# Optimization experiments

Hardware: AMD Instinct MI355X
Metric: run time of the kernel (lower is better)

The kernel has to match this reference:

```python
import jax, jax.numpy as jnp
import numpy as np

N_NODES = 50000
N_EDGES = 800000
IN = 128
HID = 128
OUT = 128
EDGE_F = 2
EPS = 1e-30


def _linear_params(key, fan_in, fan_out, bias=True):
    k1, k2 = jax.random.split(key)
    bound = 1.0 / np.sqrt(fan_in)
    W = jax.random.uniform(k1, (fan_in, fan_out), jnp.float32, -bound, bound)
    if bias:
        b = jax.random.uniform(k2, (fan_out,), jnp.float32, -bound, bound)
        return W, b
    return (W,)


def setup_inputs() -> dict:
    key = jax.random.key(0)
    ks = jax.random.split(key, 12)
    node_feat = jax.random.normal(ks[0], (N_NODES, IN), jnp.float32)
    coord_feat = jax.random.normal(ks[1], (N_NODES, 3), jnp.float32)
    edge_feat = jax.random.normal(ks[2], (N_EDGES, EDGE_F), jnp.float32)
    src = jax.random.randint(ks[3], (N_EDGES,), 0, N_NODES, jnp.int32)
    dst = jax.random.randint(ks[4], (N_EDGES,), 0, N_NODES, jnp.int32)
    # edge_mlp: Linear(2*IN+EDGE_F+1 -> HID), SiLU, Linear(HID -> HID), SiLU
    eW1, eb1 = _linear_params(ks[5], 2 * IN + EDGE_F + 1, HID)
    eW2, eb2 = _linear_params(ks[6], HID, HID)
    # node_mlp: Linear(IN+HID -> HID), SiLU, Linear(HID -> OUT)
    nW1, nb1 = _linear_params(ks[7], IN + HID, HID)
    nW2, nb2 = _linear_params(ks[8], HID, OUT)
    # coord_mlp: Linear(HID -> HID), SiLU, Linear(HID -> 1, bias=False)
    cW1, cb1 = _linear_params(ks[9], HID, HID)
    (cW2,) = _linear_params(ks[10], HID, 1, bias=False)
    return {
        "node_feat": node_feat, "coord_feat": coord_feat, "edge_feat": edge_feat,
        "src": src, "dst": dst,
        "eW1": eW1, "eb1": eb1, "eW2": eW2, "eb2": eb2,
        "nW1": nW1, "nb1": nb1, "nW2": nW2, "nb2": nb2,
        "cW1": cW1, "cb1": cb1, "cW2": cW2,
    }


def reference(node_feat, coord_feat, edge_feat, src, dst,
              eW1, eb1, eW2, eb2, nW1, nb1, nW2, nb2, cW1, cb1, cW2):
    silu = jax.nn.silu
    n = node_feat.shape[0]
    # per-edge gathers (src -> dst message flow, as in DGL)
    h_src = node_feat[src]                      # [E, IN]
    h_dst = node_feat[dst]                      # [E, IN]
    x_diff = coord_feat[src] - coord_feat[dst]  # [E, 3]
    radial = jnp.sum(x_diff * x_diff, axis=1, keepdims=True)  # [E, 1]
    x_diff = x_diff / (jnp.sqrt(radial) + EPS)
    # edge MLP
    f = jnp.concatenate([h_src, h_dst, radial, edge_feat], axis=-1)  # [E, 2*IN+1+EF]
    msg_h = silu(silu(f @ eW1 + eb1) @ eW2 + eb2)                    # [E, HID]
    msg_x = (silu(msg_h @ cW1 + cb1) @ cW2) * x_diff                 # [E, 3]
    # scatter to destination nodes: sum for h, mean for x
    h_neigh = jax.ops.segment_sum(msg_h, dst, num_segments=n)        # [N, HID]
    x_sum = jax.ops.segment_sum(msg_x, dst, num_segments=n)          # [N, 3]
    deg = jax.ops.segment_sum(jnp.ones((msg_x.shape[0],), msg_x.dtype), dst, num_segments=n)
    x_neigh = x_sum / jnp.maximum(deg, 1.0)[:, None]
    # node update
    h = silu(jnp.concatenate([node_feat, h_neigh], axis=-1) @ nW1 + nb1) @ nW2 + nb2
    x = coord_feat + x_neigh
    return h, x
```

## Files before the change

### kernel.cpp

```cpp
#include <hip/hip_runtime.h>
#include <hip/hip_bf16.h>

#define N_NODES 50000
#define E_TOTAL 800000
#define IN      128
#define HID     128
#define EPB     64
#define XOFF    ((size_t)N_NODES * HID)
#define FP      296
#define H1OFF   160
#define HP      136
#define CP      264

typedef __attribute__((ext_vector_type(8))) short short8v;
typedef __attribute__((ext_vector_type(4))) float f32x4;

__device__ __forceinline__ float silu_f(float x) { return x / (1.0f + __expf(-x)); }

__device__ __forceinline__ uint pkbf(float lo, float hi) {
    float2 f; f.x = lo; f.y = hi;
    __hip_bfloat162 h = __float22bfloat162_rn(f);
    union { __hip_bfloat162 h; uint u; } c; c.h = h;
    return c.u;
}

__device__ __forceinline__ ushort f2bf(float x) {
    uint u = __float_as_uint(x);
    u += 0x7fff + ((u >> 16) & 1);
    return (ushort)(u >> 16);
}

__device__ __forceinline__ float bf2f(short s) {
    return __uint_as_float(((uint)(ushort)s) << 16);
}

__global__ __launch_bounds__(256) void prep_kernel(
    const float* __restrict__ eW1, const float* __restrict__ eW2,
    const float* __restrict__ cW1, const float* __restrict__ nW1,
    const float* __restrict__ nW2, const float* __restrict__ eb1,
    const float* __restrict__ node_feat,
    ushort* __restrict__ pk1old, ushort* __restrict__ pka, ushort* __restrict__ pkb,
    ushort* __restrict__ pk2, ushort* __restrict__ pk3,
    ushort* __restrict__ pkn1, ushort* __restrict__ pkn2,
    float* __restrict__ cmb, ushort* __restrict__ nfb, int do_nfb)
{
    int id = blockIdx.x * 256 + threadIdx.x;
    if (id < 18944) {
        const float* W; ushort* dp; int K, idx;
        if (id < 4608)       { idx = id;         W = eW1;            dp = pk1old; K = 259; }
        else if (id < 6656)  { idx = id - 4608;  W = eW1;            dp = pka;    K = 128; }
        else if (id < 8704)  { idx = id - 6656;  W = eW1 + 128*128;  dp = pkb;    K = 128; }
        else if (id < 10752) { idx = id - 8704;  W = eW2;            dp = pk2;    K = 128; }
        else if (id < 12800) { idx = id - 10752; W = cW1;            dp = pk3;    K = 128; }
        else if (id < 16896) { idx = id - 12800; W = nW1;            dp = pkn1;   K = 256; }
        else                 { idx = id - 16896; W = nW2;            dp = pkn2;   K = 128; }
        int kt = idx >> 9, n = (idx >> 6) & 7, ll = idx & 63;
        int col = (n << 4) + (ll & 15);
        short8v o;
#pragma unroll
        for (int j = 0; j < 8; ++j) {
            int k = (kt << 5) + ((ll >> 4) << 3) + j;
            o[j] = (k < K) ? (short)f2bf(W[(size_t)k * 128 + col]) : (short)0;
        }
        *reinterpret_cast<short8v*>(dp + (size_t)idx * 8) = o;
    } else if (id < 19072) {
        int c = id - 18944;
        cmb[c*4+0] = eW1[256*128 + c];
        cmb[c*4+1] = eW1[257*128 + c];
        cmb[c*4+2] = eW1[258*128 + c];
        cmb[c*4+3] = eb1[c];
    } else if (do_nfb) {
        int idx = id - 19072;
        if (idx < N_NODES * 16) {
            const float4* s = reinterpret_cast<const float4*>(node_feat + (size_t)idx * 8);
            float4 a = s[0], b = s[1];
            uint4 u;
            u.x = pkbf(a.x, a.y); u.y = pkbf(a.z, a.w);
            u.z = pkbf(b.x, b.y); u.w = pkbf(b.z, b.w);
            *reinterpret_cast<uint4*>(nfb + (size_t)idx * 8) = u;
        }
    }
}

__global__ __launch_bounds__(256) void hist_kernel(
    const int* __restrict__ dst, int* __restrict__ cnt)
{
    int e = blockIdx.x * 256 + threadIdx.x;
    if (e < E_TOTAL) atomicAdd(&cnt[dst[e]], 1);
}

__global__ __launch_bounds__(1024) void scan_a(
    const int* __restrict__ cnt, int* __restrict__ part)
{
    __shared__ int ws[16];
    int t = threadIdx.x, lane = t & 63, wv = t >> 6;
    int i = blockIdx.x * 1024 + t;
    int v = (i < N_NODES) ? cnt[i] : 0;
#pragma unroll
    for (int off = 32; off >= 1; off >>= 1) v += __shfl_xor(v, off);
    if (lane == 0) ws[wv] = v;
    __syncthreads();
    if (t < 16) {
        int s = ws[t];
#pragma unroll
        for (int off = 8; off >= 1; off >>= 1) s += __shfl_xor(s, off);
        if (t == 0) part[blockIdx.x] = s;
    }
}

__global__ __launch_bounds__(64) void scan_b(int* __restrict__ part, int n)
{
    int t = threadIdx.x;
    int v = (t < n) ? part[t] : 0;
    int x = v;
#pragma unroll
    for (int off = 1; off < 64; off <<= 1) {
        int y = __shfl_up(x, off);
        if (t >= off) x += y;
    }
    if (t < n) part[t] = x - v;
}

__global__ __launch_bounds__(1024) void scan_c(
    int* __restrict__ cnt, const int* __restrict__ part, int* __restrict__ ptr2)
{
    __shared__ int ws[16];
    int t = threadIdx.x, lane = t & 63, wv = t >> 6;
    int i = blockIdx.x * 1024 + t;
    int v = (i < N_NODES) ? cnt[i] : 0;
    int x = v;
#pragma unroll
    for (int off = 1; off < 64; off <<= 1) {
        int y = __shfl_up(x, off);
        if (lane >= off) x += y;
    }
    if (lane == 63) ws[wv] = x;
    __syncthreads();
    if (t < 16) {
        int s = ws[t], xx = s;
#pragma unroll
        for (int off = 1; off < 16; off <<= 1) {
            int y = __shfl_up(xx, off);
            if (t >= off) xx += y;
        }
        ws[t] = xx - s;
    }
    __syncthreads();
    int excl = part[blockIdx.x] + ws[wv] + x - v;
    if (i < N_NODES) { cnt[i] = excl; ptr2[i] = excl; }
    if (i == N_NODES - 1) { cnt[N_NODES] = E_TOTAL; ptr2[N_NODES] = E_TOTAL; }
}

__global__ __launch_bounds__(256) void scatter_kernel(
    const int* __restrict__ dst, int* __restrict__ ptr2, int* __restrict__ perm)
{
    int e = blockIdx.x * 256 + threadIdx.x;
    if (e < E_TOTAL) {
        int p = atomicAdd(&ptr2[dst[e]], 1);
        perm[p] = e;
    }
}

__global__ __launch_bounds__(256) void ygemm_kernel(
    const float* __restrict__ node_feat,
    const ushort* __restrict__ pka, const ushort* __restrict__ pkb,
    ushort* __restrict__ y)
{
    __shared__ __attribute__((aligned(16))) ushort catb[32][HP];
    __shared__ __attribute__((aligned(16))) ushort ybuf[32][CP];

    const int t   = threadIdx.x;
    const int l   = t & 63;
    const int ch  = t >> 6;
    const int r16 = l & 15;
    const int g   = l >> 4;
    const int nb  = blockIdx.x * 32;

    {
        int nd = t >> 3;
        int c  = (t & 7) << 4;
        int gn = nb + nd; if (gn >= N_NODES) gn = N_NODES - 1;
        const float4* sp = reinterpret_cast<const float4*>(node_feat + (size_t)gn * 128 + c);
        float4 a = sp[0], b = sp[1], cc = sp[2], dd = sp[3];
        uint4 u0, u1;
        u0.x = pkbf(a.x, a.y);  u0.y = pkbf(a.z, a.w);
        u0.z = pkbf(b.x, b.y);  u0.w = pkbf(b.z, b.w);
        u1.x = pkbf(cc.x, cc.y); u1.y = pkbf(cc.z, cc.w);
        u1.z = pkbf(dd.x, dd.y); u1.w = pkbf(dd.z, dd.w);
        *reinterpret_cast<uint4*>(&catb[nd][c])     = u0;
        *reinterpret_cast<uint4*>(&catb[nd][c + 8]) = u1;
    }
    __syncthreads();

    const f32x4 zero = {0.f, 0.f, 0.f, 0.f};
    const short8v* pa = reinterpret_cast<const short8v*>((ch < 2) ? pka : pkb);
    const int nbase = (ch & 1) << 2;

    f32x4 acc[2][4];
#pragma unroll
    for (int et = 0; et < 2; ++et)
#pragma unroll
        for (int nt = 0; nt < 4; ++nt) acc[et][nt] = zero;

    for (int kt = 0; kt < 4; ++kt) {
        short8v b0 = *reinterpret_cast<const short8v*>(&catb[r16][(kt << 5) + (g << 3)]);
        short8v b1 = *reinterpret_cast<const short8v*>(&catb[16 + r16][(kt << 5) + (g << 3)]);
#pragma unroll
        for (int nt = 0; nt < 4; ++nt) {
            short8v a = pa[(((kt << 3) + nbase + nt) << 6) + l];
            acc[0][nt] = __builtin_amdgcn_mfma_f32_16x16x32_bf16(a, b0, acc[0][nt], 0, 0, 0);
            acc[1][nt] = __builtin_amdgcn_mfma_f32_16x16x32_bf16(a, b1, acc[1][nt], 0, 0, 0);
        }
    }
#pragma unroll
    for (int nt = 0; nt < 4; ++nt) {
        int cb = (ch << 6) + (nt << 4) + (g << 2);
#pragma unroll
        for (int et = 0; et < 2; ++et) {
            f32x4 v = acc[et][nt];
            uint2 p;
            p.x = pkbf(v[0], v[1]); p.y = pkbf(v[2], v[3]);
            *reinterpret_cast<uint2*>(&ybuf[(et << 4) + r16][cb]) = p;
        }
    }
    __syncthreads();

#pragma unroll
    for (int i = 0; i < 4; ++i) {
        int idx = t + (i << 8);
        int nd  = idx >> 5;
        int c16 = (idx & 31) << 3;
        int gn  = nb + nd;
        if (gn < N_NODES)
            *reinterpret_cast<short8v*>(y + (size_t)gn * 256 + c16) =
                *reinterpret_cast<const short8v*>(&ybuf[nd][c16]);
    }
}

__global__ __launch_bounds__(512, 4) void edge2_kernel(
    const ushort* __restrict__ y, const float* __restrict__ coord,
    const float* __restrict__ edge_feat,
    const int* __restrict__ src, const int* __restrict__ dst,
    const int* __restrict__ perm,
    const float* __restrict__ cmb,
    const ushort* __restrict__ pk2, const ushort* __restrict__ pk3,
    const float* __restrict__ eb2,
    const float* __restrict__ cb1, const float* __restrict__ cW2,
    float* __restrict__ hacc, float* __restrict__ xacc)
{
    __shared__ __attribute__((aligned(16))) ushort h1buf[EPB][HP];
    __shared__ __attribute__((aligned(16))) ushort msgbuf[EPB][HP];
    __shared__ int   sbuf[EPB], dbuf[EPB];
    __shared__ float xdbuf[EPB][4];
    __shared__ float rbuf[EPB][4];
    __shared__ float pbuf[4][EPB];

    const int t   = threadIdx.x;
    const int l   = t & 63;
    const int w   = t >> 6;
    const int ch  = w & 3;
    const int eh  = w >> 2;
    const int r16 = l & 15;
    const int g   = l >> 4;
    const int e_base = blockIdx.x * EPB;

    if (t < EPB) {
        int ee = perm[e_base + t];
        int s = src[ee], d = dst[ee];
        sbuf[t] = s; dbuf[t] = d;
        float dx = coord[(size_t)s*3+0] - coord[(size_t)d*3+0];
        float dy = coord[(size_t)s*3+1] - coord[(size_t)d*3+1];
        float dz = coord[(size_t)s*3+2] - coord[(size_t)d*3+2];
        float radial = dx*dx + dy*dy + dz*dz;
        float inv = 1.0f / (sqrtf(radial) + 1e-30f);
        xdbuf[t][0] = dx * inv; xdbuf[t][1] = dy * inv; xdbuf[t][2] = dz * inv;
        rbuf[t][0] = radial;
        rbuf[t][1] = edge_feat[(size_t)ee*2 + 0];
        rbuf[t][2] = edge_feat[(size_t)ee*2 + 1];
    }
    __syncthreads();

    {
        const int c = (t & 15) << 3;
        const float4* cmb4 = reinterpret_cast<const float4*>(cmb);
#pragma unroll
        for (int p = 0; p < 2; ++p) {
            int e = (t >> 4) + (p << 5);
            short8v a8 = *reinterpret_cast<const short8v*>(y + (size_t)sbuf[e] * 256 + c);
            short8v b8 = *reinterpret_cast<const short8v*>(y + (size_t)dbuf[e] * 256 + 128 + c);
            float r = rbuf[e][0], f0 = rbuf[e][1], f1 = rbuf[e][2];
            float vv[8];
#pragma unroll
            for (int j = 0; j < 8; ++j) {
                float4 q = cmb4[c + j];
                float s = bf2f(a8[j]) + bf2f(b8[j]) + r*q.x + f0*q.y + f1*q.z + q.w;
                vv[j] = silu_f(s);
            }
            uint4 u;
            u.x = pkbf(vv[0], vv[1]); u.y = pkbf(vv[2], vv[3]);
            u.z = pkbf(vv[4], vv[5]); u.w = pkbf(vv[6], vv[7]);
            *reinterpret_cast<uint4*>(&h1buf[e][c]) = u;
        }
    }
    __syncthreads();

    const f32x4 zero = {0.f, 0.f, 0.f, 0.f};
    const short8v* pkv2 = reinterpret_cast<const short8v*>(pk2);
    const short8v* pkv3 = reinterpret_cast<const short8v*>(pk3);

    f32x4 acc[2][2];
    acc[0][0] = zero; acc[0][1] = zero; acc[1][0] = zero; acc[1][1] = zero;
    for (int kt = 0; kt < 4; ++kt) {
        short8v b0 = *reinterpret_cast<const short8v*>(&h1buf[(eh << 5) + r16][(kt << 5) + (g << 3)]);
        short8v b1 = *reinterpret_cast<const short8v*>(&h1buf[(eh << 5) + 16 + r16][(kt << 5) + (g << 3)]);
#pragma unroll
        for (int nt = 0; nt < 2; ++nt) {
            short8v a = pkv2[(((kt << 3) + (ch << 1) + nt) << 6) + l];
            acc[0][nt] = __builtin_amdgcn_mfma_f32_16x16x32_bf16(a, b0, acc[0][nt], 0, 0, 0);
            acc[1][nt] = __builtin_amdgcn_mfma_f32_16x16x32_bf16(a, b1, acc[1][nt], 0, 0, 0);
        }
    }
#pragma unroll
    for (int nt = 0; nt < 2; ++nt) {
        int cb = (ch << 5) + (nt << 4) + (g << 2);
        float4 bias = *reinterpret_cast<const float4*>(&eb2[cb]);
#pragma unroll
        for (int et = 0; et < 2; ++et) {
            int e = (eh << 5) + (et << 4) + r16;
            f32x4 v = acc[et][nt];
            uint2 p;
            p.x = pkbf(silu_f(v[0] + bias.x), silu_f(v[1] + bias.y));
            p.y = pkbf(silu_f(v[2] + bias.z), silu_f(v[3] + bias.w));
            *reinterpret_cast<uint2*>(&msgbuf[e][cb]) = p;
        }
    }
    __syncthreads();

    {
        const int c = t & 127;
        const int q = t >> 7;
        float sum = 0.f;
        int cur = dbuf[q << 4];
#pragma unroll
        for (int i = 0; i < 16; ++i) {
            int e = (q << 4) + i;
            sum += __uint_as_float((uint)msgbuf[e][c] << 16);
            int nxt = (i < 15) ? dbuf[e + 1] : -1;
            if (nxt != cur) {
                atomicAdd(&hacc[(size_t)cur * HID + c], sum);
                sum = 0.f; cur = nxt;
            }
        }
    }

    acc[0][0] = zero; acc[0][1] = zero; acc[1][0] = zero; acc[1][1] = zero;
    for (int kt = 0; kt < 4; ++kt) {
        short8v b0 = *reinterpret_cast<const short8v*>(&msgbuf[(eh << 5) + r16][(kt << 5) + (g << 3)]);
        short8v b1 = *reinterpret_cast<const short8v*>(&msgbuf[(eh << 5) + 16 + r16][(kt << 5) + (g << 3)]);
#pragma unroll
        for (int nt = 0; nt < 2; ++nt) {
            short8v a = pkv3[(((kt << 3) + (ch << 1) + nt) << 6) + l];
            acc[0][nt] = __builtin_amdgcn_mfma_f32_16x16x32_bf16(a, b0, acc[0][nt], 0, 0, 0);
            acc[1][nt] = __builtin_amdgcn_mfma_f32_16x16x32_bf16(a, b1, acc[1][nt], 0, 0, 0);
        }
    }
    float part[2] = {0.f, 0.f};
#pragma unroll
    for (int nt = 0; nt < 2; ++nt) {
        int cb = (ch << 5) + (nt << 4) + (g << 2);
        float4 bias = *reinterpret_cast<const float4*>(&cb1[cb]);
        float4 cw   = *reinterpret_cast<const float4*>(&cW2[cb]);
#pragma unroll
        for (int et = 0; et < 2; ++et) {
            f32x4 v = acc[et][nt];
            part[et] += silu_f(v[0] + bias.x) * cw.x + silu_f(v[1] + bias.y) * cw.y
                      + silu_f(v[2] + bias.z) * cw.z + silu_f(v[3] + bias.w) * cw.w;
        }
    }
#pragma unroll
    for (int et = 0; et < 2; ++et) {
        part[et] += __shfl_xor(part[et], 16);
        part[et] += __shfl_xor(part[et], 32);
    }
    if (l < 16) {
        pbuf[ch][(eh << 5) + r16]      = part[0];
        pbuf[ch][(eh << 5) + 16 + r16] = part[1];
    }
    __syncthreads();

    if (t < EPB) {
        float s = pbuf[0][t] + pbuf[1][t] + pbuf[2][t] + pbuf[3][t];
        int gd = dbuf[t];
        atomicAdd(&xacc[(size_t)gd*3 + 0], s * xdbuf[t][0]);
        atomicAdd(&xacc[(size_t)gd*3 + 1], s * xdbuf[t][1]);
        atomicAdd(&xacc[(size_t)gd*3 + 2], s * xdbuf[t][2]);
    }
}

template<bool NFB>
__global__ __launch_bounds__(512, 8) void edge_kernel(
    const float* __restrict__ node_feat, const ushort* __restrict__ nfb,
    const float* __restrict__ coord, const float* __restrict__ edge_feat,
    const int* __restrict__ src, const int* __restrict__ dst,
    const int* __restrict__ perm, int use_perm,
    const ushort* __restrict__ pk1, const ushort* __restrict__ pk2,
    const ushort* __restrict__ pk3,
    const float* __restrict__ eb1, const float* __restrict__ eb2,
    const float* __restrict__ cb1, const float* __restrict__ cW2,
    float* __restrict__ hacc, float* __restrict__ xacc)
{
    __shared__ __attribute__((aligned(16))) ushort fbuf[EPB][FP];
    __shared__ int   sbuf[EPB], dbuf[EPB];
    __shared__ float xdbuf[EPB][4];
    __shared__ float pbuf[4][EPB];

    const int t   = threadIdx.x;
    const int l   = t & 63;
    const int w   = t >> 6;
    const int ch  = w & 3;
    const int eh  = w >> 2;
    const int r16 = l & 15;
    const int g   = l >> 4;
    const int e_base = blockIdx.x * EPB;

    int ee = 0;
    if (t < EPB) {
        ee = use_perm ? perm[e_base + t] : (e_base + t);
        sbuf[t] = src[ee];
        dbuf[t] = dst[ee];
    }
    __syncthreads();

    {
        const int e = t >> 3;
        const int c = (t & 7) << 5;
        if (NFB) {
            const ushort* sp = (c < 128) ? nfb + (size_t)sbuf[e] * 128 + c
                                         : nfb + (size_t)dbuf[e] * 128 + (c - 128);
            const short8v* spv = reinterpret_cast<const short8v*>(sp);
#pragma unroll
            for (int i = 0; i < 4; ++i)
                *reinterpret_cast<short8v*>(&fbuf[e][c + (i << 3)]) = spv[i];
        } else {
            const float* sp = (c < 128) ? node_feat + (size_t)sbuf[e] * 128 + c
                                        : node_feat + (size_t)dbuf[e] * 128 + (c - 128);
            const float4* spv = reinterpret_cast<const float4*>(sp);
#pragma unroll
            for (int i = 0; i < 4; ++i) {
                float4 a = spv[2 * i], b = spv[2 * i + 1];
                uint4 u;
                u.x = pkbf(a.x, a.y); u.y = pkbf(a.z, a.w);
                u.z = pkbf(b.x, b.y); u.w = pkbf(b.z, b.w);
                *reinterpret_cast<uint4*>(&fbuf[e][c + (i << 3)]) = u;
            }
        }
    }
    if (t < EPB) {
        const int e = t, s = sbuf[e], d = dbuf[e];
        float dx = coord[(size_t)s*3+0] - coord[(size_t)d*3+0];
        float dy = coord[(size_t)s*3+1] - coord[(size_t)d*3+1];
        float dz = coord[(size_t)s*3+2] - coord[(size_t)d*3+2];
        float radial = dx*dx + dy*dy + dz*dz;
        float inv = 1.0f / (sqrtf(radial) + 1e-30f);
        fbuf[e][256] = f2bf(radial);
        fbuf[e][257] = f2bf(edge_feat[(size_t)ee*2 + 0]);
        fbuf[e][258] = f2bf(edge_feat[(size_t)ee*2 + 1]);
#pragma unroll
        for (int k = 259; k < 288; ++k) fbuf[e][k] = 0;
        xdbuf[e][0] = dx * inv; xdbuf[e][1] = dy * inv; xdbuf[e][2] = dz * inv;
    }
    __syncthreads();

    const f32x4 zero = {0.f, 0.f, 0.f, 0.f};
    const short8v* pkv1 = reinterpret_cast<const short8v*>(pk1);
    const short8v* pkv2 = reinterpret_cast<const short8v*>(pk2);
    const short8v* pkv3 = reinterpret_cast<const short8v*>(pk3);

    f32x4 acc[2][2];
    acc[0][0] = zero; acc[0][1] = zero; acc[1][0] = zero; acc[1][1] = zero;
    for (int kt = 0; kt < 9; ++kt) {
        short8v b0 = *reinterpret_cast<const short8v*>(&fbuf[(eh << 5) + r16][(kt << 5) + (g << 3)]);
        short8v b1 = *reinterpret_cast<const short8v*>(&fbuf[(eh << 5) + 16 + r16][(kt << 5) + (g << 3)]);
#pragma unroll
        for (int nt = 0; nt < 2; ++nt) {
            short8v a = pkv1[(((kt << 3) + (ch << 1) + nt) << 6) + l];
            acc[0][nt] = __builtin_amdgcn_mfma_f32_16x16x32_bf16(a, b0, acc[0][nt], 0, 0, 0);
            acc[1][nt] = __builtin_amdgcn_mfma_f32_16x16x32_bf16(a, b1, acc[1][nt], 0, 0, 0);
        }
    }
    __syncthreads();
#pragma unroll
    for (int nt = 0; nt < 2; ++nt) {
        int cb = (ch << 5) + (nt << 4) + (g << 2);
        float4 bias = *reinterpret_cast<const float4*>(&eb1[cb]);
#pragma unroll
        for (int et = 0; et < 2; ++et) {
            int e = (eh << 5) + (et << 4) + r16;
            f32x4 v = acc[et][nt];
            uint2 p;
            p.x = pkbf(silu_f(v[0] + bias.x), silu_f(v[1] + bias.y));
            p.y = pkbf(silu_f(v[2] + bias.z), silu_f(v[3] + bias.w));
            *reinterpret_cast<uint2*>(&fbuf[e][H1OFF + cb]) = p;
        }
    }
    __syncthreads();

    acc[0][0] = zero; acc[0][1] = zero; acc[1][0] = zero; acc[1][1] = zero;
    for (int kt = 0; kt < 4; ++kt) {
        short8v b0 = *reinterpret_cast<const short8v*>(&fbuf[(eh << 5) + r16][H1OFF + (kt << 5) + (g << 3)]);
        short8v b1 = *reinterpret_cast<const short8v*>(&fbuf[(eh << 5) + 16 + r16][H1OFF + (kt << 5) + (g << 3)]);
#pragma unroll
        for (int nt = 0; nt < 2; ++nt) {
            short8v a = pkv2[(((kt << 3) + (ch << 1) + nt) << 6) + l];
            acc[0][nt] = __builtin_amdgcn_mfma_f32_16x16x32_bf16(a, b0, acc[0][nt], 0, 0, 0);
            acc[1][nt] = __builtin_amdgcn_mfma_f32_16x16x32_bf16(a, b1, acc[1][nt], 0, 0, 0);
        }
    }
#pragma unroll
    for (int nt = 0; nt < 2; ++nt) {
        int cb = (ch << 5) + (nt << 4) + (g << 2);
        float4 bias = *reinterpret_cast<const float4*>(&eb2[cb]);
#pragma unroll
        for (int et = 0; et < 2; ++et) {
            int e = (eh << 5) + (et << 4) + r16;
            f32x4 v = acc[et][nt];
            uint2 p;
            p.x = pkbf(silu_f(v[0] + bias.x), silu_f(v[1] + bias.y));
            p.y = pkbf(silu_f(v[2] + bias.z), silu_f(v[3] + bias.w));
            *reinterpret_cast<uint2*>(&fbuf[e][cb]) = p;
        }
    }
    __syncthreads();

    {
        const int c = t & 127;
        const int q = t >> 7;
        float sum = 0.f;
        int cur = dbuf[q << 4];
#pragma unroll
        for (int i = 0; i < 16; ++i) {
            int e = (q << 4) + i;
            sum += __uint_as_float((uint)fbuf[e][c] << 16);
            int nxt = (i < 15) ? dbuf[e + 1] : -1;
            if (nxt != cur) {
                atomicAdd(&hacc[(size_t)cur * HID + c], sum);
                sum = 0.f; cur = nxt;
            }
        }
    }

    acc[0][0] = zero; acc[0][1] = zero; acc[1][0] = zero; acc[1][1] = zero;
    for (int kt = 0; kt < 4; ++kt) {
        short8v b0 = *reinterpret_cast<const short8v*>(&fbuf[(eh << 5) + r16][(kt << 5) + (g << 3)]);
        short8v b1 = *reinterpret_cast<const short8v*>(&fbuf[(eh << 5) + 16 + r16][(kt << 5) + (g << 3)]);
#pragma unroll
        for (int nt = 0; nt < 2; ++nt) {
            short8v a = pkv3[(((kt << 3) + (ch << 1) + nt) << 6) + l];
            acc[0][nt] = __builtin_amdgcn_mfma_f32_16x16x32_bf16(a, b0, acc[0][nt], 0, 0, 0);
            acc[1][nt] = __builtin_amdgcn_mfma_f32_16x16x32_bf16(a, b1, acc[1][nt], 0, 0, 0);
        }
    }
    float part[2] = {0.f, 0.f};
#pragma unroll
    for (int nt = 0; nt < 2; ++nt) {
        int cb = (ch << 5) + (nt << 4) + (g << 2);
        float4 bias = *reinterpret_cast<const float4*>(&cb1[cb]);
        float4 cw   = *reinterpret_cast<const float4*>(&cW2[cb]);
#pragma unroll
        for (int et = 0; et < 2; ++et) {
            f32x4 v = acc[et][nt];
            part[et] += silu_f(v[0] + bias.x) * cw.x + silu_f(v[1] + bias.y) * cw.y
                      + silu_f(v[2] + bias.z) * cw.z + silu_f(v[3] + bias.w) * cw.w;
        }
    }
#pragma unroll
    for (int et = 0; et < 2; ++et) {
        part[et] += __shfl_xor(part[et], 16);
        part[et] += __shfl_xor(part[et], 32);
    }
    if (l < 16) {
        pbuf[ch][(eh << 5) + r16]      = part[0];
        pbuf[ch][(eh << 5) + 16 + r16] = part[1];
    }
    __syncthreads();

    if (t < EPB) {
        float s = pbuf[0][t] + pbuf[1][t] + pbuf[2][t] + pbuf[3][t];
        int gd = dbuf[t];
        atomicAdd(&xacc[(size_t)gd*3 + 0], s * xdbuf[t][0]);
        atomicAdd(&xacc[(size_t)gd*3 + 1], s * xdbuf[t][1]);
        atomicAdd(&xacc[(size_t)gd*3 + 2], s * xdbuf[t][2]);
    }
}

template<bool NFB>
__global__ __launch_bounds__(256) void node_kernel(
    const float* __restrict__ node_feat, const ushort* __restrict__ nfb,
    const float* __restrict__ coord,
    const ushort* __restrict__ pkn1, const ushort* __restrict__ pkn2,
    const float* __restrict__ nb1, const float* __restrict__ nb2,
    float* __restrict__ dout, const int* __restrict__ ptr)
{
    __shared__ __attribute__((aligned(16))) ushort catb[32][CP];
    __shared__ __attribute__((aligned(16))) ushort h1b[32][HP];

    const int t   = threadIdx.x;
    const int l   = t & 63;
    const int w   = t >> 6;
    const int ch  = w & 1;
    const int eh  = w >> 1;
    const int r16 = l & 15;
    const int g   = l >> 4;
    const int nb  = blockIdx.x * 32;

    {
        int nd = t >> 3;
        int c  = (t & 7) << 5;
        int gn = nb + nd; if (gn >= N_NODES) gn = N_NODES - 1;
        if (c < 128) {
            if (NFB) {
                const short8v* spv = reinterpret_cast<const short8v*>(nfb + (size_t)gn * 128 + c);
#pragma unroll
                for (int i = 0; i < 4; ++i)
                    *reinterpret_cast<short8v*>(&catb[nd][c + (i << 3)]) = spv[i];
            } else {
                const float4* spv = reinterpret_cast<const float4*>(node_feat + (size_t)gn * 128 + c);
#pragma unroll
                for (int i = 0; i < 4; ++i) {
                    float4 a = spv[2 * i], b = spv[2 * i + 1];
                    uint4 u;
                    u.x = pkbf(a.x, a.y); u.y = pkbf(a.z, a.w);
                    u.z = pkbf(b.x, b.y); u.w = pkbf(b.z, b.w);
                    *reinterpret_cast<uint4*>(&catb[nd][c + (i << 3)]) = u;
                }
            }
        } else {
            const float4* spv = reinterpret_cast<const float4*>(dout + (size_t)gn * HID + (c - 128));
#pragma unroll
            for (int i = 0; i < 4; ++i) {
                float4 a = spv[2 * i], b = spv[2 * i + 1];
                uint4 u;
                u.x = pkbf(a.x, a.y); u.y = pkbf(a.z, a.w);
                u.z = pkbf(b.x, b.y); u.w = pkbf(b.z, b.w);
                *reinterpret_cast<uint4*>(&catb[nd][c + (i << 3)]) = u;
            }
        }
    }
    __syncthreads();

    const f32x4 zero = {0.f, 0.f, 0.f, 0.f};
    const short8v* pv1 = reinterpret_cast<const short8v*>(pkn1);
    const short8v* pv2 = reinterpret_cast<const short8v*>(pkn2);

    f32x4 acc[4];
#pragma unroll
    for (int nt = 0; nt < 4; ++nt) acc[nt] = zero;
    for (int kt = 0; kt < 8; ++kt) {
        short8v b = *reinterpret_cast<const short8v*>(&catb[(eh << 4) + r16][(kt << 5) + (g << 3)]);
#pragma unroll
        for (int nt = 0; nt < 4; ++nt) {
            short8v a = pv1[(((kt << 3) + (ch << 2) + nt) << 6) + l];
            acc[nt] = __builtin_amdgcn_mfma_f32_16x16x32_bf16(a, b, acc[nt], 0, 0, 0);
        }
    }
#pragma unroll
    for (int nt = 0; nt < 4; ++nt) {
        int cb = (ch << 6) + (nt << 4) + (g << 2);
        float4 bias = *reinterpret_cast<const float4*>(&nb1[cb]);
        int nd = (eh << 4) + r16;
        f32x4 v = acc[nt];
        uint2 p;
        p.x = pkbf(silu_f(v[0] + bias.x), silu_f(v[1] + bias.y));
        p.y = pkbf(silu_f(v[2] + bias.z), silu_f(v[3] + bias.w));
        *reinterpret_cast<uint2*>(&h1b[nd][cb]) = p;
    }
    __syncthreads();

#pragma unroll
    for (int nt = 0; nt < 4; ++nt) acc[nt] = zero;
    for (int kt = 0; kt < 4; ++kt) {
        short8v b = *reinterpret_cast<const short8v*>(&h1b[(eh << 4) + r16][(kt << 5) + (g << 3)]);
#pragma unroll
        for (int nt = 0; nt < 4; ++nt) {
            short8v a = pv2[(((kt << 3) + (ch << 2) + nt) << 6) + l];
            acc[nt] = __builtin_amdgcn_mfma_f32_16x16x32_bf16(a, b, acc[nt], 0, 0, 0);
        }
    }
    {
        int gw = nb + (eh << 4) + r16;
        if (gw < N_NODES) {
#pragma unroll
            for (int nt = 0; nt < 4; ++nt) {
                int cb = (ch << 6) + (nt << 4) + (g << 2);
                float4 bias = *reinterpret_cast<const float4*>(&nb2[cb]);
                f32x4 v = acc[nt];
                float4 o;
                o.x = v[0] + bias.x; o.y = v[1] + bias.y;
                o.z = v[2] + bias.z; o.w = v[3] + bias.w;
                *reinterpret_cast<float4*>(&dout[(size_t)gw * HID + cb]) = o;
            }
        }
    }

    if (t < 96) {
        int nd = t / 3, d = t - 3 * nd;
        int gn = nb + nd;
        if (gn < N_NODES) {
            size_t xi = XOFF + (size_t)gn * 3 + d;
            float dg = (float)(ptr[gn + 1] - ptr[gn]);
            dg = dg > 1.0f ? dg : 1.0f;
            dout[xi] = coord[(size_t)gn * 3 + d] + dout[xi] / dg;
        }
    }
}

extern "C" void kernel_launch(void* const* d_in, const int* in_sizes, int n_in,
                              void* d_out, int out_size, void* d_ws, size_t ws_size,
                              hipStream_t stream) {
    const float* node_feat = (const float*)d_in[0];
    const float* coord     = (const float*)d_in[1];
    const float* edge_feat = (const float*)d_in[2];
    const int*   src       = (const int*)d_in[3];
    const int*   dst       = (const int*)d_in[4];
    const float* eW1 = (const float*)d_in[5];
    const float* eb1 = (const float*)d_in[6];
    const float* eW2 = (const float*)d_in[7];
    const float* eb2 = (const float*)d_in[8];
    const float* nW1 = (const float*)d_in[9];
    const float* nb1 = (const float*)d_in[10];
    const float* nW2 = (const float*)d_in[11];
    const float* nb2 = (const float*)d_in[12];
    const float* cW1 = (const float*)d_in[13];
    const float* cb1 = (const float*)d_in[14];
    const float* cW2 = (const float*)d_in[15];

    float* out = (float*)d_out;
    char* base = (char*)d_ws;
    int*    ptrb   = (int*)base;
    int*    part   = (int*)(base + 200064);
    int*    ptr2   = (int*)(base + 200320);
    ushort* pk1old = (ushort*)(base + 400384);
    ushort* pka    = (ushort*)(base + 474112);
    ushort* pkb    = (ushort*)(base + 506880);
    ushort* pk2    = (ushort*)(base + 539648);
    ushort* pk3    = (ushort*)(base + 572416);
    ushort* pkn1   = (ushort*)(base + 605184);
    ushort* pkn2   = (ushort*)(base + 670720);
    float*  cmb    = (float*)(base + 703488);
    int*    perm   = (int*)(base + 705536);
    ushort* ybuf   = (ushort*)(base + 3905536);
    const size_t need_y    = 3905536 + (size_t)N_NODES * 256 * 2;
    const size_t need_nfb  = 3905536 + (size_t)N_NODES * 128 * 2;
    const size_t need_perm = 3905536;
    const bool use_y    = ws_size >= need_y;
    const bool use_nfb  = !use_y && ws_size >= need_nfb;
    const bool use_perm = ws_size >= need_perm;

    hipMemsetAsync(d_out, 0, (size_t)out_size * sizeof(float), stream);
    hipMemsetAsync(d_ws, 0, 200064, stream);

    int prep_grid = (use_nfb ? (19072 + N_NODES * 16) + 255 : 19072 + 255) / 256;
    prep_kernel<<<prep_grid, 256, 0, stream>>>(
        eW1, eW2, cW1, nW1, nW2, eb1, node_feat,
        pk1old, pka, pkb, pk2, pk3, pkn1, pkn2, cmb, ybuf, use_nfb ? 1 : 0);

    hist_kernel<<<(E_TOTAL + 255) / 256, 256, 0, stream>>>(dst, ptrb);
    scan_a<<<49, 1024, 0, stream>>>(ptrb, part);
    scan_b<<<1, 64, 0, stream>>>(part, 49);
    scan_c<<<49, 1024, 0, stream>>>(ptrb, part, ptr2);
    if (use_perm)
        scatter_kernel<<<(E_TOTAL + 255) / 256, 256, 0, stream>>>(dst, ptr2, perm);

    if (use_y) {
        ygemm_kernel<<<(N_NODES + 31) / 32, 256, 0, stream>>>(node_feat, pka, pkb, ybuf);
        edge2_kernel<<<E_TOTAL / EPB, 512, 0, stream>>>(
            ybuf, coord, edge_feat, src, dst, perm, cmb,
            pk2, pk3, eb2, cb1, cW2, out, out + XOFF);
        node_kernel<false><<<(N_NODES + 31) / 32, 256, 0, stream>>>(
            node_feat, ybuf, coord, pkn1, pkn2, nb1, nb2, out, ptrb);
    } else if (use_nfb) {
        edge_kernel<true><<<E_TOTAL / EPB, 512, 0, stream>>>(
            node_feat, ybuf, coord, edge_feat, src, dst, perm, use_perm ? 1 : 0,
            pk1old, pk2, pk3, eb1, eb2, cb1, cW2, out, out + XOFF);
        node_kernel<true><<<(N_NODES + 31) / 32, 256, 0, stream>>>(
            node_feat, ybuf, coord, pkn1, pkn2, nb1, nb2, out, ptrb);
    } else {
        edge_kernel<false><<<E_TOTAL / EPB, 512, 0, stream>>>(
            node_feat, ybuf, coord, edge_feat, src, dst, perm, use_perm ? 1 : 0,
            pk1old, pk2, pk3, eb1, eb2, cb1, cW2, out, out + XOFF);
        node_kernel<false><<<(N_NODES + 31) / 32, 256, 0, stream>>>(
            node_feat, ybuf, coord, pkn1, pkn2, nb1, nb2, out, ptrb);
    }
}
```

Before: 523.6 us.

## Process 128 edges per block, share one LDS buffer, fold eb1 into node GEMM

The edge kernel now handles 128 dst-sorted edges per 1024-thread block instead of 64 per 512 threads. The h1 and message staging buffers are merged into a single LDS buffer, with an extra barrier between the reads and the overwrite. The first-layer bias eb1 is now added once per node in the y GEMM epilogue instead of once per edge, and the per-edge pre-activation uses explicit FMAs. Larger blocks give longer same-destination runs, so fewer atomics are issued per segment, but each block has more threads to synchronise at every barrier.

```diff
diff --git a/kernel.cpp b/kernel.cpp
--- a/kernel.cpp
+++ b/kernel.cpp
@@ -6,6 +6,7 @@
 #define IN      128
 #define HID     128
 #define EPB     64
+#define EPB2    128
 #define XOFF    ((size_t)N_NODES * HID)
 #define FP      296
 #define H1OFF   160
@@ -164,6 +165,7 @@
 __global__ __launch_bounds__(256) void ygemm_kernel(
     const float* __restrict__ node_feat,
     const ushort* __restrict__ pka, const ushort* __restrict__ pkb,
+    const float* __restrict__ eb1,
     ushort* __restrict__ y)
 {
     __shared__ __attribute__((aligned(16))) ushort catb[32][HP];
@@ -215,11 +217,14 @@
 #pragma unroll
     for (int nt = 0; nt < 4; ++nt) {
         int cb = (ch << 6) + (nt << 4) + (g << 2);
+        float4 bias = {0.f, 0.f, 0.f, 0.f};
+        if (ch < 2) bias = *reinterpret_cast<const float4*>(&eb1[cb]);
 #pragma unroll
         for (int et = 0; et < 2; ++et) {
             f32x4 v = acc[et][nt];
             uint2 p;
-            p.x = pkbf(v[0], v[1]); p.y = pkbf(v[2], v[3]);
+            p.x = pkbf(v[0] + bias.x, v[1] + bias.y);
+            p.y = pkbf(v[2] + bias.z, v[3] + bias.w);
             *reinterpret_cast<uint2*>(&ybuf[(et << 4) + r16][cb]) = p;
         }
     }
@@ -237,7 +242,7 @@
     }
 }
 
-__global__ __launch_bounds__(512, 4) void edge2_kernel(
+__global__ __launch_bounds__(1024, 2) void edge2_kernel(
     const ushort* __restrict__ y, const float* __restrict__ coord,
     const float* __restrict__ edge_feat,
     const int* __restrict__ src, const int* __restrict__ dst,
@@ -248,12 +253,11 @@
     const float* __restrict__ cb1, const float* __restrict__ cW2,
     float* __restrict__ hacc, float* __restrict__ xacc)
 {
-    __shared__ __attribute__((aligned(16))) ushort h1buf[EPB][HP];
-    __shared__ __attribute__((aligned(16))) ushort msgbuf[EPB][HP];
-    __shared__ int   sbuf[EPB], dbuf[EPB];
-    __shared__ float xdbuf[EPB][4];
-    __shared__ float rbuf[EPB][4];
-    __shared__ float pbuf[4][EPB];
+    __shared__ __attribute__((aligned(16))) ushort ebuf[EPB2][HP];
+    __shared__ int   sbuf[EPB2], dbuf[EPB2];
+    __shared__ float xdbuf[EPB2][4];
+    __shared__ float rbuf[EPB2][4];
+    __shared__ float pbuf[4][EPB2];
 
     const int t   = threadIdx.x;
     const int l   = t & 63;
@@ -262,9 +266,9 @@
     const int eh  = w >> 2;
     const int r16 = l & 15;
     const int g   = l >> 4;
-    const int e_base = blockIdx.x * EPB;
-
-    if (t < EPB) {
+    const int e_base = blockIdx.x * EPB2;
+
+    if (t < EPB2) {
         int ee = perm[e_base + t];
         int s = src[ee], d = dst[ee];
         sbuf[t] = s; dbuf[t] = d;
@@ -285,7 +289,7 @@
         const float4* cmb4 = reinterpret_cast<const float4*>(cmb);
 #pragma unroll
         for (int p = 0; p < 2; ++p) {
-            int e = (t >> 4) + (p << 5);
+            int e = (t >> 4) + (p << 6);
             short8v a8 = *reinterpret_cast<const short8v*>(y + (size_t)sbuf[e] * 256 + c);
             short8v b8 = *reinterpret_cast<const short8v*>(y + (size_t)dbuf[e] * 256 + 128 + c);
             float r = rbuf[e][0], f0 = rbuf[e][1], f1 = rbuf[e][2];
@@ -293,13 +297,16 @@
 #pragma unroll
             for (int j = 0; j < 8; ++j) {
                 float4 q = cmb4[c + j];
-                float s = bf2f(a8[j]) + bf2f(b8[j]) + r*q.x + f0*q.y + f1*q.z + q.w;
+                float s = bf2f(a8[j]) + bf2f(b8[j]);
+                s = fmaf(r, q.x, s);
+                s = fmaf(f0, q.y, s);
+                s = fmaf(f1, q.z, s);
                 vv[j] = silu_f(s);
             }
             uint4 u;
             u.x = pkbf(vv[0], vv[1]); u.y = pkbf(vv[2], vv[3]);
             u.z = pkbf(vv[4], vv[5]); u.w = pkbf(vv[6], vv[7]);
-            *reinterpret_cast<uint4*>(&h1buf[e][c]) = u;
+            *reinterpret_cast<uint4*>(&ebuf[e][c]) = u;
         }
     }
     __syncthreads();
@@ -311,8 +318,8 @@
     f32x4 acc[2][2];
     acc[0][0] = zero; acc[0][1] = zero; acc[1][0] = zero; acc[1][1] = zero;
     for (int kt = 0; kt < 4; ++kt) {
-        short8v b0 = *reinterpret_cast<const short8v*>(&h1buf[(eh << 5) + r16][(kt << 5) + (g << 3)]);
-        short8v b1 = *reinterpret_cast<const short8v*>(&h1buf[(eh << 5) + 16 + r16][(kt << 5) + (g << 3)]);
+        short8v b0 = *reinterpret_cast<const short8v*>(&ebuf[(eh << 5) + r16][(kt << 5) + (g << 3)]);
+        short8v b1 = *reinterpret_cast<const short8v*>(&ebuf[(eh << 5) + 16 + r16][(kt << 5) + (g << 3)]);
 #pragma unroll
         for (int nt = 0; nt < 2; ++nt) {
             short8v a = pkv2[(((kt << 3) + (ch << 1) + nt) << 6) + l];
@@ -320,6 +327,8 @@
             acc[1][nt] = __builtin_amdgcn_mfma_f32_16x16x32_bf16(a, b1, acc[1][nt], 0, 0, 0);
         }
     }
+    __syncthreads();
+
 #pragma unroll
     for (int nt = 0; nt < 2; ++nt) {
         int cb = (ch << 5) + (nt << 4) + (g << 2);
@@ -331,7 +340,7 @@
             uint2 p;
             p.x = pkbf(silu_f(v[0] + bias.x), silu_f(v[1] + bias.y));
             p.y = pkbf(silu_f(v[2] + bias.z), silu_f(v[3] + bias.w));
-            *reinterpret_cast<uint2*>(&msgbuf[e][cb]) = p;
+            *reinterpret_cast<uint2*>(&ebuf[e][cb]) = p;
         }
     }
     __syncthreads();
@@ -344,7 +353,7 @@
 #pragma unroll
         for (int i = 0; i < 16; ++i) {
             int e = (q << 4) + i;
-            sum += __uint_as_float((uint)msgbuf[e][c] << 16);
+            sum += __uint_as_float((uint)ebuf[e][c] << 16);
             int nxt = (i < 15) ? dbuf[e + 1] : -1;
             if (nxt != cur) {
                 atomicAdd(&hacc[(size_t)cur * HID + c], sum);
@@ -355,8 +364,8 @@
 
     acc[0][0] = zero; acc[0][1] = zero; acc[1][0] = zero; acc[1][1] = zero;
     for (int kt = 0; kt < 4; ++kt) {
-        short8v b0 = *reinterpret_cast<const short8v*>(&msgbuf[(eh << 5) + r16][(kt << 5) + (g << 3)]);
-        short8v b1 = *reinterpret_cast<const short8v*>(&msgbuf[(eh << 5) + 16 + r16][(kt << 5) + (g << 3)]);
+        short8v b0 = *reinterpret_cast<const short8v*>(&ebuf[(eh << 5) + r16][(kt << 5) + (g << 3)]);
+        short8v b1 = *reinterpret_cast<const short8v*>(&ebuf[(eh << 5) + 16 + r16][(kt << 5) + (g << 3)]);
 #pragma unroll
         for (int nt = 0; nt < 2; ++nt) {
             short8v a = pkv3[(((kt << 3) + (ch << 1) + nt) << 6) + l];
@@ -388,7 +397,7 @@
     }
     __syncthreads();
 
-    if (t < EPB) {
+    if (t < EPB2) {
         float s = pbuf[0][t] + pbuf[1][t] + pbuf[2][t] + pbuf[3][t];
         int gd = dbuf[t];
         atomicAdd(&xacc[(size_t)gd*3 + 0], s * xdbuf[t][0]);
@@ -772,8 +781,8 @@
         scatter_kernel<<<(E_TOTAL + 255) / 256, 256, 0, stream>>>(dst, ptr2, perm);
 
     if (use_y) {
-        ygemm_kernel<<<(N_NODES + 31) / 32, 256, 0, stream>>>(node_feat, pka, pkb, ybuf);
-        edge2_kernel<<<E_TOTAL / EPB, 512, 0, stream>>>(
+        ygemm_kernel<<<(N_NODES + 31) / 32, 256, 0, stream>>>(node_feat, pka, pkb, eb1, ybuf);
+        edge2_kernel<<<E_TOTAL / EPB2, 1024, 0, stream>>>(
             ybuf, coord, edge_feat, src, dst, perm, cmb,
             pk2, pk3, eb2, cb1, cW2, out, out + XOFF);
         node_kernel<false><<<(N_NODES + 31) / 32, 256, 0, stream>>>(
```

Result: slower. 716.1 us (+36.8%).

## Precompute sorted per-edge records in scatter and fold edge bias into ygemm

Applied to the files above, without the earlier changes.

The scatter pass now also writes a 32-byte record per edge in destination-sorted order. Each record holds src, dst, the edge features, the radial distance and the normalized coordinate difference. The edge kernel reads these records directly, which removes the dependent perm→src/dst→coord gather chain and one barrier from its prologue. The first-layer bias eb1 is added into the precomputed y table, so the per-edge loop no longer adds it, and the h segment reduction now handles two bf16 channels per 32-bit load. In exchange it needs an extra 25.6 MB of workspace, more write traffic in scatter, and only takes the new path when the workspace is large enough.

```diff
diff --git a/kernel.cpp b/kernel.cpp
--- a/kernel.cpp
+++ b/kernel.cpp
@@ -152,18 +152,37 @@
 }
 
 __global__ __launch_bounds__(256) void scatter_kernel(
-    const int* __restrict__ dst, int* __restrict__ ptr2, int* __restrict__ perm)
+    const int* __restrict__ dst, const int* __restrict__ src,
+    const float* __restrict__ edge_feat, const float* __restrict__ coord,
+    int* __restrict__ ptr2, int* __restrict__ perm,
+    float4* __restrict__ rec, int use_rec)
 {
     int e = blockIdx.x * 256 + threadIdx.x;
-    if (e < E_TOTAL) {
-        int p = atomicAdd(&ptr2[dst[e]], 1);
-        perm[p] = e;
+    if (e >= E_TOTAL) return;
+    int d = dst[e];
+    int p = atomicAdd(&ptr2[d], 1);
+    perm[p] = e;
+    if (use_rec) {
+        int s = src[e];
+        float dx = coord[(size_t)s*3+0] - coord[(size_t)d*3+0];
+        float dy = coord[(size_t)s*3+1] - coord[(size_t)d*3+1];
+        float dz = coord[(size_t)s*3+2] - coord[(size_t)d*3+2];
+        float radial = dx*dx + dy*dy + dz*dz;
+        float inv = 1.0f / (sqrtf(radial) + 1e-30f);
+        float2 ef = *reinterpret_cast<const float2*>(&edge_feat[(size_t)e*2]);
+        float4 ra, rb;
+        ra.x = __int_as_float(s); ra.y = __int_as_float(d);
+        ra.z = ef.x; ra.w = ef.y;
+        rb.x = radial; rb.y = dx*inv; rb.z = dy*inv; rb.w = dz*inv;
+        rec[(size_t)p*2]   = ra;
+        rec[(size_t)p*2+1] = rb;
     }
 }
 
 __global__ __launch_bounds__(256) void ygemm_kernel(
     const float* __restrict__ node_feat,
     const ushort* __restrict__ pka, const ushort* __restrict__ pkb,
+    const float* __restrict__ eb1,
     ushort* __restrict__ y)
 {
     __shared__ __attribute__((aligned(16))) ushort catb[32][HP];
@@ -215,11 +234,14 @@
 #pragma unroll
     for (int nt = 0; nt < 4; ++nt) {
         int cb = (ch << 6) + (nt << 4) + (g << 2);
+        float4 bias = {0.f, 0.f, 0.f, 0.f};
+        if (ch < 2) bias = *reinterpret_cast<const float4*>(&eb1[cb]);
 #pragma unroll
         for (int et = 0; et < 2; ++et) {
             f32x4 v = acc[et][nt];
             uint2 p;
-            p.x = pkbf(v[0], v[1]); p.y = pkbf(v[2], v[3]);
+            p.x = pkbf(v[0] + bias.x, v[1] + bias.y);
+            p.y = pkbf(v[2] + bias.z, v[3] + bias.w);
             *reinterpret_cast<uint2*>(&ybuf[(et << 4) + r16][cb]) = p;
         }
     }
@@ -237,11 +259,12 @@
     }
 }
 
+template<int REC>
 __global__ __launch_bounds__(512, 4) void edge2_kernel(
     const ushort* __restrict__ y, const float* __restrict__ coord,
     const float* __restrict__ edge_feat,
     const int* __restrict__ src, const int* __restrict__ dst,
-    const int* __restrict__ perm,
+    const int* __restrict__ perm, const float4* __restrict__ rec,
     const float* __restrict__ cmb,
     const ushort* __restrict__ pk2, const ushort* __restrict__ pk3,
     const float* __restrict__ eb2,
@@ -264,23 +287,57 @@
     const int g   = l >> 4;
     const int e_base = blockIdx.x * EPB;
 
-    if (t < EPB) {
-        int ee = perm[e_base + t];
-        int s = src[ee], d = dst[ee];
-        sbuf[t] = s; dbuf[t] = d;
-        float dx = coord[(size_t)s*3+0] - coord[(size_t)d*3+0];
-        float dy = coord[(size_t)s*3+1] - coord[(size_t)d*3+1];
-        float dz = coord[(size_t)s*3+2] - coord[(size_t)d*3+2];
-        float radial = dx*dx + dy*dy + dz*dz;
-        float inv = 1.0f / (sqrtf(radial) + 1e-30f);
-        xdbuf[t][0] = dx * inv; xdbuf[t][1] = dy * inv; xdbuf[t][2] = dz * inv;
-        rbuf[t][0] = radial;
-        rbuf[t][1] = edge_feat[(size_t)ee*2 + 0];
-        rbuf[t][2] = edge_feat[(size_t)ee*2 + 1];
-    }
-    __syncthreads();
-
-    {
+    if (REC) {
+        if (t < EPB) {
+            float4 ra = rec[(size_t)(e_base + t) * 2];
+            float4 rb = rec[(size_t)(e_base + t) * 2 + 1];
+            sbuf[t] = __float_as_int(ra.x);
+            dbuf[t] = __float_as_int(ra.y);
+            xdbuf[t][0] = rb.y; xdbuf[t][1] = rb.z; xdbuf[t][2] = rb.w;
+        }
+        const int c = (t & 15) << 3;
+        const float4* cmb4 = reinterpret_cast<const float4*>(cmb);
+#pragma unroll
+        for (int p = 0; p < 2; ++p) {
+            int e = (t >> 4) + (p << 5);
+            size_t ge = (size_t)(e_base + e);
+            float4 ra = rec[ge * 2];
+            float4 rb = rec[ge * 2 + 1];
+            int s = __float_as_int(ra.x), d = __float_as_int(ra.y);
+            short8v a8 = *reinterpret_cast<const short8v*>(y + (size_t)s * 256 + c);
+            short8v b8 = *reinterpret_cast<const short8v*>(y + (size_t)d * 256 + 128 + c);
+            float r = rb.x, f0 = ra.z, f1 = ra.w;
+            float vv[8];
+#pragma unroll
+            for (int j = 0; j < 8; ++j) {
+                float4 q = cmb4[c + j];
+                float sv = bf2f(a8[j]) + bf2f(b8[j]);
+                sv = fmaf(r, q.x, sv);
+                sv = fmaf(f0, q.y, sv);
+                sv = fmaf(f1, q.z, sv);
+                vv[j] = silu_f(sv);
+            }
+            uint4 u;
+            u.x = pkbf(vv[0], vv[1]); u.y = pkbf(vv[2], vv[3]);
+            u.z = pkbf(vv[4], vv[5]); u.w = pkbf(vv[6], vv[7]);
+            *reinterpret_cast<uint4*>(&h1buf[e][c]) = u;
+        }
+    } else {
+        if (t < EPB) {
+            int ee = perm[e_base + t];
+            int s = src[ee], d = dst[ee];
+            sbuf[t] = s; dbuf[t] = d;
+            float dx = coord[(size_t)s*3+0] - coord[(size_t)d*3+0];
+            float dy = coord[(size_t)s*3+1] - coord[(size_t)d*3+1];
+            float dz = coord[(size_t)s*3+2] - coord[(size_t)d*3+2];
+            float radial = dx*dx + dy*dy + dz*dz;
+            float inv = 1.0f / (sqrtf(radial) + 1e-30f);
+            xdbuf[t][0] = dx * inv; xdbuf[t][1] = dy * inv; xdbuf[t][2] = dz * inv;
+            rbuf[t][0] = radial;
+            rbuf[t][1] = edge_feat[(size_t)ee*2 + 0];
+            rbuf[t][2] = edge_feat[(size_t)ee*2 + 1];
+        }
+        __syncthreads();
         const int c = (t & 15) << 3;
         const float4* cmb4 = reinterpret_cast<const float4*>(cmb);
 #pragma unroll
@@ -293,8 +350,11 @@
 #pragma unroll
             for (int j = 0; j < 8; ++j) {
                 float4 q = cmb4[c + j];
-                float s = bf2f(a8[j]) + bf2f(b8[j]) + r*q.x + f0*q.y + f1*q.z + q.w;
-                vv[j] = silu_f(s);
+                float sv = bf2f(a8[j]) + bf2f(b8[j]);
+                sv = fmaf(r, q.x, sv);
+                sv = fmaf(f0, q.y, sv);
+                sv = fmaf(f1, q.z, sv);
+                vv[j] = silu_f(sv);
             }
             uint4 u;
             u.x = pkbf(vv[0], vv[1]); u.y = pkbf(vv[2], vv[3]);
@@ -337,18 +397,22 @@
     __syncthreads();
 
     {
-        const int c = t & 127;
-        const int q = t >> 7;
-        float sum = 0.f;
-        int cur = dbuf[q << 4];
-#pragma unroll
-        for (int i = 0; i < 16; ++i) {
-            int e = (q << 4) + i;
-            sum += __uint_as_float((uint)msgbuf[e][c] << 16);
-            int nxt = (i < 15) ? dbuf[e + 1] : -1;
+        const int c2 = t & 63;
+        const int q  = t >> 6;
+        float s0 = 0.f, s1 = 0.f;
+        int cur = dbuf[q << 3];
+#pragma unroll
+        for (int i = 0; i < 8; ++i) {
+            int e = (q << 3) + i;
+            uint v = *reinterpret_cast<const uint*>(&msgbuf[e][c2 << 1]);
+            s0 += __uint_as_float(v << 16);
+            s1 += __uint_as_float(v & 0xffff0000u);
+            int nxt = (i < 7) ? dbuf[e + 1] : -1;
             if (nxt != cur) {
-                atomicAdd(&hacc[(size_t)cur * HID + c], sum);
-                sum = 0.f; cur = nxt;
+                float* dp = &hacc[(size_t)cur * HID + (c2 << 1)];
+                atomicAdd(dp,     s0);
+                atomicAdd(dp + 1, s1);
+                s0 = 0.f; s1 = 0.f; cur = nxt;
             }
         }
     }
@@ -749,10 +813,13 @@
     float*  cmb    = (float*)(base + 703488);
     int*    perm   = (int*)(base + 705536);
     ushort* ybuf   = (ushort*)(base + 3905536);
+    float4* rec    = (float4*)(base + 29505536);
+    const size_t need_rec  = 29505536 + (size_t)E_TOTAL * 32;
     const size_t need_y    = 3905536 + (size_t)N_NODES * 256 * 2;
     const size_t need_nfb  = 3905536 + (size_t)N_NODES * 128 * 2;
     const size_t need_perm = 3905536;
     const bool use_y    = ws_size >= need_y;
+    const bool use_rec  = use_y && ws_size >= need_rec;
     const bool use_nfb  = !use_y && ws_size >= need_nfb;
     const bool use_perm = ws_size >= need_perm;
 
@@ -769,13 +836,20 @@
     scan_b<<<1, 64, 0, stream>>>(part, 49);
     scan_c<<<49, 1024, 0, stream>>>(ptrb, part, ptr2);
     if (use_perm)
-        scatter_kernel<<<(E_TOTAL + 255) / 256, 256, 0, stream>>>(dst, ptr2, perm);
+        scatter_kernel<<<(E_TOTAL + 255) / 256, 256, 0, stream>>>(
+            dst, src, edge_feat, coord, ptr2, perm, rec, use_rec ? 1 : 0);
 
     if (use_y) {
-        ygemm_kernel<<<(N_NODES + 31) / 32, 256, 0, stream>>>(node_feat, pka, pkb, ybuf);
-        edge2_kernel<<<E_TOTAL / EPB, 512, 0, stream>>>(
-            ybuf, coord, edge_feat, src, dst, perm, cmb,
-            pk2, pk3, eb2, cb1, cW2, out, out + XOFF);
+        ygemm_kernel<<<(N_NODES + 31) / 32, 256, 0, stream>>>(node_feat, pka, pkb, eb1, ybuf);
+        if (use_rec) {
+            edge2_kernel<1><<<E_TOTAL / EPB, 512, 0, stream>>>(
+                ybuf, coord, edge_feat, src, dst, perm, rec, cmb,
+                pk2, pk3, eb2, cb1, cW2, out, out + XOFF);
+        } else {
+            edge2_kernel<0><<<E_TOTAL / EPB, 512, 0, stream>>>(
+                ybuf, coord, edge_feat, src, dst, perm, rec, cmb,
+                pk2, pk3, eb2, cb1, cW2, out, out + XOFF);
+        }
         node_kernel<false><<<(N_NODES + 31) / 32, 256, 0, stream>>>(
             node_feat, ybuf, coord, pkn1, pkn2, nb1, nb2, out, ptrb);
     } else if (use_nfb) {
```

After: 613.8 us. +17.2%, slower.

## Fuse preprocessing kernels to cut launches and fold eb1 into ygemm

Applied to the files above, without the earlier changes.

Folds the degree histogram into the weight-packing kernel, moves the middle scan step into the final scan kernel, and runs the edge scatter and the per-node y GEMM inside one launch by splitting blocks by index. It also adds bias eb1 in the y GEMM epilogue so the edge kernel no longer adds it per element, and uses explicit FMAs. The aim is to remove several small kernel launches and their serialization gaps, plus some per-edge arithmetic. In exchange, bias is rounded to bf16 together with y, which slightly changes numerics. If use_perm were false, ygemm would not run while use_y is set, but the defaults take the perm path.

```diff
diff --git a/kernel.cpp b/kernel.cpp
--- a/kernel.cpp
+++ b/kernel.cpp
@@ -34,11 +34,12 @@
     return __uint_as_float(((uint)(ushort)s) << 16);
 }
 
-__global__ __launch_bounds__(256) void prep_kernel(
+__global__ __launch_bounds__(256) void prep_hist_kernel(
     const float* __restrict__ eW1, const float* __restrict__ eW2,
     const float* __restrict__ cW1, const float* __restrict__ nW1,
     const float* __restrict__ nW2, const float* __restrict__ eb1,
-    const float* __restrict__ node_feat,
+    const float* __restrict__ node_feat, const int* __restrict__ dst,
+    int* __restrict__ cnt,
     ushort* __restrict__ pk1old, ushort* __restrict__ pka, ushort* __restrict__ pkb,
     ushort* __restrict__ pk2, ushort* __restrict__ pk3,
     ushort* __restrict__ pkn1, ushort* __restrict__ pkn2,
@@ -69,8 +70,12 @@
         cmb[c*4+1] = eW1[257*128 + c];
         cmb[c*4+2] = eW1[258*128 + c];
         cmb[c*4+3] = eb1[c];
+    } else if (id < 19200) {
+    } else if (id < 19200 + E_TOTAL) {
+        int e = id - 19200;
+        atomicAdd(&cnt[dst[e]], 1);
     } else if (do_nfb) {
-        int idx = id - 19072;
+        int idx = id - 19200 - E_TOTAL;
         if (idx < N_NODES * 16) {
             const float4* s = reinterpret_cast<const float4*>(node_feat + (size_t)idx * 8);
             float4 a = s[0], b = s[1];
@@ -82,13 +87,6 @@
     }
 }
 
-__global__ __launch_bounds__(256) void hist_kernel(
-    const int* __restrict__ dst, int* __restrict__ cnt)
-{
-    int e = blockIdx.x * 256 + threadIdx.x;
-    if (e < E_TOTAL) atomicAdd(&cnt[dst[e]], 1);
-}
-
 __global__ __launch_bounds__(1024) void scan_a(
     const int* __restrict__ cnt, int* __restrict__ part)
 {
@@ -108,24 +106,26 @@
     }
 }
 
-__global__ __launch_bounds__(64) void scan_b(int* __restrict__ part, int n)
-{
-    int t = threadIdx.x;
-    int v = (t < n) ? part[t] : 0;
-    int x = v;
-#pragma unroll
-    for (int off = 1; off < 64; off <<= 1) {
-        int y = __shfl_up(x, off);
-        if (t >= off) x += y;
-    }
-    if (t < n) part[t] = x - v;
-}
-
-__global__ __launch_bounds__(1024) void scan_c(
+__global__ __launch_bounds__(1024) void scan_c2(
     int* __restrict__ cnt, const int* __restrict__ part, int* __restrict__ ptr2)
 {
     __shared__ int ws[16];
+    __shared__ int base_s;
     int t = threadIdx.x, lane = t & 63, wv = t >> 6;
+
+    if (t < 64) {
+        int pv = (t < 49) ? part[t] : 0;
+        int px = pv;
+#pragma unroll
+        for (int off = 1; off < 64; off <<= 1) {
+            int y = __shfl_up(px, off);
+            if (t >= off) px += y;
+        }
+        int b = blockIdx.x;
+        if (b == 0) { if (t == 0) base_s = 0; }
+        else        { if (t == b - 1) base_s = px; }
+    }
+
     int i = blockIdx.x * 1024 + t;
     int v = (i < N_NODES) ? cnt[i] : 0;
     int x = v;
@@ -146,35 +146,35 @@
         ws[t] = xx - s;
     }
     __syncthreads();
-    int excl = part[blockIdx.x] + ws[wv] + x - v;
+    int excl = base_s + ws[wv] + x - v;
     if (i < N_NODES) { cnt[i] = excl; ptr2[i] = excl; }
     if (i == N_NODES - 1) { cnt[N_NODES] = E_TOTAL; ptr2[N_NODES] = E_TOTAL; }
 }
 
-__global__ __launch_bounds__(256) void scatter_kernel(
-    const int* __restrict__ dst, int* __restrict__ ptr2, int* __restrict__ perm)
-{
-    int e = blockIdx.x * 256 + threadIdx.x;
-    if (e < E_TOTAL) {
-        int p = atomicAdd(&ptr2[dst[e]], 1);
-        perm[p] = e;
-    }
-}
-
-__global__ __launch_bounds__(256) void ygemm_kernel(
+__global__ __launch_bounds__(256) void scat_ygemm_kernel(
+    const int* __restrict__ dst, int* __restrict__ ptr2, int* __restrict__ perm,
     const float* __restrict__ node_feat,
     const ushort* __restrict__ pka, const ushort* __restrict__ pkb,
-    ushort* __restrict__ y)
+    const float* __restrict__ eb1, ushort* __restrict__ y)
 {
     __shared__ __attribute__((aligned(16))) ushort catb[32][HP];
     __shared__ __attribute__((aligned(16))) ushort ybuf[32][CP];
+
+    if (blockIdx.x < 3125) {
+        int e = blockIdx.x * 256 + threadIdx.x;
+        if (e < E_TOTAL) {
+            int p = atomicAdd(&ptr2[dst[e]], 1);
+            perm[p] = e;
+        }
+        return;
+    }
 
     const int t   = threadIdx.x;
     const int l   = t & 63;
     const int ch  = t >> 6;
     const int r16 = l & 15;
     const int g   = l >> 4;
-    const int nb  = blockIdx.x * 32;
+    const int nb  = (blockIdx.x - 3125) * 32;
 
     {
         int nd = t >> 3;
@@ -215,11 +215,14 @@
 #pragma unroll
     for (int nt = 0; nt < 4; ++nt) {
         int cb = (ch << 6) + (nt << 4) + (g << 2);
+        float4 bias = {0.f, 0.f, 0.f, 0.f};
+        if (ch < 2) bias = *reinterpret_cast<const float4*>(&eb1[cb]);
 #pragma unroll
         for (int et = 0; et < 2; ++et) {
             f32x4 v = acc[et][nt];
             uint2 p;
-            p.x = pkbf(v[0], v[1]); p.y = pkbf(v[2], v[3]);
+            p.x = pkbf(v[0] + bias.x, v[1] + bias.y);
+            p.y = pkbf(v[2] + bias.z, v[3] + bias.w);
             *reinterpret_cast<uint2*>(&ybuf[(et << 4) + r16][cb]) = p;
         }
     }
@@ -293,8 +296,11 @@
 #pragma unroll
             for (int j = 0; j < 8; ++j) {
                 float4 q = cmb4[c + j];
-                float s = bf2f(a8[j]) + bf2f(b8[j]) + r*q.x + f0*q.y + f1*q.z + q.w;
-                vv[j] = silu_f(s);
+                float sv = bf2f(a8[j]) + bf2f(b8[j]);
+                sv = fmaf(r, q.x, sv);
+                sv = fmaf(f0, q.y, sv);
+                sv = fmaf(f1, q.z, sv);
+                vv[j] = silu_f(sv);
             }
             uint4 u;
             u.x = pkbf(vv[0], vv[1]); u.y = pkbf(vv[2], vv[3]);
@@ -759,20 +765,21 @@
     hipMemsetAsync(d_out, 0, (size_t)out_size * sizeof(float), stream);
     hipMemsetAsync(d_ws, 0, 200064, stream);
 
-    int prep_grid = (use_nfb ? (19072 + N_NODES * 16) + 255 : 19072 + 255) / 256;
-    prep_kernel<<<prep_grid, 256, 0, stream>>>(
-        eW1, eW2, cW1, nW1, nW2, eb1, node_feat,
+    int ph_ids = 19200 + E_TOTAL + (use_nfb ? N_NODES * 16 : 0);
+    prep_hist_kernel<<<(ph_ids + 255) / 256, 256, 0, stream>>>(
+        eW1, eW2, cW1, nW1, nW2, eb1, node_feat, dst, ptrb,
         pk1old, pka, pkb, pk2, pk3, pkn1, pkn2, cmb, ybuf, use_nfb ? 1 : 0);
 
-    hist_kernel<<<(E_TOTAL + 255) / 256, 256, 0, stream>>>(dst, ptrb);
     scan_a<<<49, 1024, 0, stream>>>(ptrb, part);
-    scan_b<<<1, 64, 0, stream>>>(part, 49);
-    scan_c<<<49, 1024, 0, stream>>>(ptrb, part, ptr2);
-    if (use_perm)
-        scatter_kernel<<<(E_TOTAL + 255) / 256, 256, 0, stream>>>(dst, ptr2, perm);
+    scan_c2<<<49, 1024, 0, stream>>>(ptrb, part, ptr2);
+
+    if (use_perm) {
+        int yg_blocks = use_y ? (N_NODES + 31) / 32 : 0;
+        scat_ygemm_kernel<<<3125 + yg_blocks, 256, 0, stream>>>(
+            dst, ptr2, perm, node_feat, pka, pkb, eb1, ybuf);
+    }
 
     if (use_y) {
-        ygemm_kernel<<<(N_NODES + 31) / 32, 256, 0, stream>>>(node_feat, pka, pkb, ybuf);
         edge2_kernel<<<E_TOTAL / EPB, 512, 0, stream>>>(
             ybuf, coord, edge_feat, src, dst, perm, cmb,
             pk2, pk3, eb2, cb1, cW2, out, out + XOFF);
```

New measurement: 602.7 us. 15.1% more time.
